# Performance work log

Measured on AMD Instinct MI355X. Metric: run time of the kernel, lower is better.

Reference implementation:

```python
import jax, jax.numpy as jnp
import numpy as np

B, S = 128, 524288  # batch, seq_len; S % target_len == 0 so rounded boundaries are uniform


def setup_inputs() -> dict:
    key = jax.random.key(0)
    x = jax.random.normal(key, (B, S), dtype=jnp.float32)
    return {"x": x, "target_len": 256}


def reference(x, target_len):
    # Original loops over target_len segments with boundaries
    # start=round(i*S/target_len), end=round((i+1)*S/target_len).
    # With S % target_len == 0 these are exactly uniform with L = S // target_len
    # (>1), so each segment's change strength is mean(|diff|) over L-1 gaps.
    b, s = x.shape
    L = s // target_len  # segment length (2048 here)
    seg = x.reshape(b, target_len, L)            # [B, T, L]
    d = jnp.abs(jnp.diff(seg, axis=2))           # [B, T, L-1]
    return d.mean(axis=2)                        # [B, T]
```

## Files before the change

### kernel.cpp

```cpp
#include <hip/hip_runtime.h>

#define SEG_LEN 2048
#define GAPS_INV (1.0f / 2047.0f)

__global__ __launch_bounds__(256)
void seg_change_strength_kernel(const float* __restrict__ x,
                                float* __restrict__ out) {
    const int t = threadIdx.x;
    const long long segBase = (long long)blockIdx.x * SEG_LEN;
    const float* p = x + segBase + (long long)t * 8;

    const float4 v0 = *(const float4*)(p);
    const float4 v1 = *(const float4*)(p + 4);
    const float nxt = (t < 255) ? p[8] : v1.w;

    float s = fabsf(v0.y - v0.x) + fabsf(v0.z - v0.y) + fabsf(v0.w - v0.z)
            + fabsf(v1.x - v0.w) + fabsf(v1.y - v1.x) + fabsf(v1.z - v1.y)
            + fabsf(v1.w - v1.z) + fabsf(nxt  - v1.w);

    #pragma unroll
    for (int off = 32; off > 0; off >>= 1)
        s += __shfl_down(s, off, 64);

    __shared__ float wsum[4];
    if ((t & 63) == 0) wsum[t >> 6] = s;
    __syncthreads();
    if (t == 0)
        out[blockIdx.x] = (wsum[0] + wsum[1] + wsum[2] + wsum[3]) * GAPS_INV;
}

extern "C" void kernel_launch(void* const* d_in, const int* in_sizes, int n_in,
                              void* d_out, int out_size, void* d_ws, size_t ws_size,
                              hipStream_t stream) {
    const float* x = (const float*)d_in[0];
    float* out = (float*)d_out;
    const int n = in_sizes[0];
    const int nseg = n / SEG_LEN;
    seg_change_strength_kernel<<<nseg, 256, 0, stream>>>(x, out);
}
```

Baseline: 345.0 us.

## Assign one wavefront per segment with coalesced strided float4 loads

Each 64-lane wavefront now reduces a whole 2048-element segment in eight coalesced float4 sweeps. Boundary gaps are handled with lane shuffles and a carry value, and each block covers four segments. This drops the shared-memory cross-wave reduction and __syncthreads, and removes the redundant scalar load of the next element. The cost is extra shuffle instructions per iteration and a quarter as many blocks, so there is less parallelism to hide memory latency.

```diff
diff --git a/kernel.cpp b/kernel.cpp
--- a/kernel.cpp
+++ b/kernel.cpp
@@ -6,27 +6,28 @@
 __global__ __launch_bounds__(256)
 void seg_change_strength_kernel(const float* __restrict__ x,
                                 float* __restrict__ out) {
-    const int t = threadIdx.x;
-    const long long segBase = (long long)blockIdx.x * SEG_LEN;
-    const float* p = x + segBase + (long long)t * 8;
+    const int lane = threadIdx.x & 63;
+    const int waveInBlock = threadIdx.x >> 6;
+    const int seg = (blockIdx.x << 2) + waveInBlock;
+    const float* base = x + (long long)seg * SEG_LEN + lane * 4;
 
-    const float4 v0 = *(const float4*)(p);
-    const float4 v1 = *(const float4*)(p + 4);
-    const float nxt = (t < 255) ? p[8] : v1.w;
-
-    float s = fabsf(v0.y - v0.x) + fabsf(v0.z - v0.y) + fabsf(v0.w - v0.z)
-            + fabsf(v1.x - v0.w) + fabsf(v1.y - v1.x) + fabsf(v1.z - v1.y)
-            + fabsf(v1.w - v1.z) + fabsf(nxt  - v1.w);
+    float s = 0.0f;
+    float carry = 0.0f;
+    #pragma unroll
+    for (int j = 0; j < 8; ++j) {
+        const float4 v = *(const float4*)(base + j * 256);
+        float sl = fabsf(v.y - v.x) + fabsf(v.z - v.y) + fabsf(v.w - v.z);
+        const float nx = __shfl_down(v.x, 1, 64);
+        if (lane < 63) sl += fabsf(nx - v.w);
+        if (j > 0 && lane == 0) sl += fabsf(v.x - carry);
+        s += sl;
+        carry = __shfl(v.w, 63, 64);
+    }
 
     #pragma unroll
     for (int off = 32; off > 0; off >>= 1)
         s += __shfl_down(s, off, 64);
-
-    __shared__ float wsum[4];
-    if ((t & 63) == 0) wsum[t >> 6] = s;
-    __syncthreads();
-    if (t == 0)
-        out[blockIdx.x] = (wsum[0] + wsum[1] + wsum[2] + wsum[3]) * GAPS_INV;
+    if (lane == 0) out[seg] = s * GAPS_INV;
 }
 
 extern "C" void kernel_launch(void* const* d_in, const int* in_sizes, int n_in,
@@ -36,5 +37,5 @@
     float* out = (float*)d_out;
     const int n = in_sizes[0];
     const int nseg = n / SEG_LEN;
-    seg_change_strength_kernel<<<nseg, 256, 0, stream>>>(x, out);
+    seg_change_strength_kernel<<<nseg / 4, 256, 0, stream>>>(x, out);
 }
```

Result: no change. 351.9 us (+2.0%).
